# Optimization experiments

Hardware: AMD Instinct MI355X
Metric: run time of the kernel (lower is better)

Reference implementation:

```python
import jax, jax.numpy as jnp
import numpy as np

B, L, D = 4, 4096, 768

def setup_inputs() -> dict:
    key = jax.random.key(0)
    ks = jax.random.split(key, 4)
    s = 1.0 / np.sqrt(D)
    return {
        "hidden_states": jax.random.normal(ks[0], (B, L, D), dtype=jnp.float32),
        "Wq": jax.random.normal(ks[1], (D, D), dtype=jnp.float32) * s,
        "bq": jnp.zeros((D,), dtype=jnp.float32),
        "Wk": jax.random.normal(ks[2], (D, D), dtype=jnp.float32) * s,
        "bk": jnp.zeros((D,), dtype=jnp.float32),
        "Wv": jax.random.normal(ks[3], (D, D), dtype=jnp.float32) * s,
        "bv": jnp.zeros((D,), dtype=jnp.float32),
    }

def reference(hidden_states, Wq, bq, Wk, bk, Wv, bv):
    # Linear projections (torch Linear: x @ W^T + b; here W stored as [in, out]-equivalent via transpose-free einsum)
    q = jnp.einsum('bld,de->ble', hidden_states, Wq) + bq
    k = jnp.einsum('bld,de->ble', hidden_states, Wk) + bk
    v = jnp.einsum('bld,de->ble', hidden_states, Wv) + bv
    # Single-head attention, NO 1/sqrt(d) scaling (faithful to source)
    weight = jnp.einsum('bqd,bkd->bqk', q, k)          # [B, L, L]
    weight = jax.nn.softmax(weight, axis=-1)
    score = jnp.einsum('bqk,bkd->bqd', weight, v)      # [B, L, D]
    return score
```

## Files before the change

### kernel.cpp

```cpp
#include <hip/hip_runtime.h>


typedef _Float16 f16;
typedef _Float16 f16x8 __attribute__((ext_vector_type(8)));
typedef _Float16 f16x4 __attribute__((ext_vector_type(4)));
typedef float f32x4 __attribute__((ext_vector_type(4)));

#define NB 4
#define NL 4096
#define ND 768
#define NM (NB * NL)

__device__ __forceinline__ void split_f16(float v, f16& h, f16& l) {
    h = (f16)v;
    l = (f16)(v - (float)h);
}

__global__ __launch_bounds__(256) void k_convert_x(
    const float* __restrict__ x, f16* __restrict__ xh, f16* __restrict__ xl) {
    int i = blockIdx.x * 256 + threadIdx.x;
    float4 v = ((const float4*)x)[i];
    float vv[4] = {v.x, v.y, v.z, v.w};
    f16x4 hv, lv;
    for (int j = 0; j < 4; ++j) {
        f16 h, l; split_f16(vv[j], h, l);
        hv[j] = h; lv[j] = l;
    }
    ((f16x4*)xh)[i] = hv;
    ((f16x4*)xl)[i] = lv;
}

__global__ __launch_bounds__(256) void k_convert_w(
    const float* __restrict__ Wq, const float* __restrict__ Wk,
    const float* __restrict__ Wv, f16* __restrict__ wth, f16* __restrict__ wtl) {
    __shared__ float tile[32][33];
    const float* W = blockIdx.z == 0 ? Wq : (blockIdx.z == 1 ? Wk : Wv);
    f16* th = wth + blockIdx.z * ND * ND;
    f16* tl = wtl + blockIdx.z * ND * ND;
    const int k0 = blockIdx.x * 32, n0 = blockIdx.y * 32;
    const int tx = threadIdx.x & 31, ty = threadIdx.x >> 5;
    for (int r = 0; r < 4; ++r)
        tile[r * 8 + ty][tx] = W[(k0 + r * 8 + ty) * ND + n0 + tx];
    __syncthreads();
    for (int r = 0; r < 4; ++r) {
        float v = tile[tx][r * 8 + ty];
        int n = n0 + r * 8 + ty, k = k0 + tx;
        f16 h, l; split_f16(v, h, l);
        th[n * ND + k] = h;
        tl[n * ND + k] = l;
    }
}

__global__ __launch_bounds__(256, 2) void k_proj(
    const f16* __restrict__ xh, const f16* __restrict__ xl,
    const f16* __restrict__ wth, const f16* __restrict__ wtl,
    const float* __restrict__ bq, const float* __restrict__ bk,
    const float* __restrict__ bv,
    f16* __restrict__ qh, f16* __restrict__ kh, f16* __restrict__ vt) {
    const int z = blockIdx.z;
    const f16* wh = wth + z * ND * ND;
    const f16* wl = wtl + z * ND * ND;
    const float* bias = z == 0 ? bq : (z == 1 ? bk : bv);
    const int m0 = blockIdx.x * 128, n0 = blockIdx.y * 128;

    __shared__ f16 Ah[128 * 40], Al[128 * 40], Bh[128 * 40], Bl[128 * 40];

    const int t = threadIdx.x;
    const int lane = t & 63, quad = lane >> 4, l16 = lane & 15;
    const int wave = t >> 6, wm = wave >> 1, wn = wave & 1;

    f32x4 acc[4][4] = {};

    for (int kt = 0; kt < 24; ++kt) {
        const int k0 = kt * 32;
        __syncthreads();
        for (int i = 0; i < 2; ++i) {
            int c = i * 256 + t;
            int row = c >> 2, kc = (c & 3) * 8;
            *(uint4*)&Ah[row * 40 + kc] = *(const uint4*)&xh[(m0 + row) * ND + k0 + kc];
            *(uint4*)&Al[row * 40 + kc] = *(const uint4*)&xl[(m0 + row) * ND + k0 + kc];
            *(uint4*)&Bh[row * 40 + kc] = *(const uint4*)&wh[(n0 + row) * ND + k0 + kc];
            *(uint4*)&Bl[row * 40 + kc] = *(const uint4*)&wl[(n0 + row) * ND + k0 + kc];
        }
        __syncthreads();
        f16x8 ah[4], al[4], bh[4], bl[4];
#pragma unroll
        for (int f = 0; f < 4; ++f) {
            int m = wm * 64 + f * 16 + l16;
            ah[f] = *(const f16x8*)&Ah[m * 40 + quad * 8];
            al[f] = *(const f16x8*)&Al[m * 40 + quad * 8];
            int n = wn * 64 + f * 16 + l16;
            bh[f] = *(const f16x8*)&Bh[n * 40 + quad * 8];
            bl[f] = *(const f16x8*)&Bl[n * 40 + quad * 8];
        }
#pragma unroll
        for (int fm = 0; fm < 4; ++fm)
#pragma unroll
            for (int fn = 0; fn < 4; ++fn) {
                f32x4 c = acc[fm][fn];
                c = __builtin_amdgcn_mfma_f32_16x16x32_f16(al[fm], bh[fn], c, 0, 0, 0);
                c = __builtin_amdgcn_mfma_f32_16x16x32_f16(ah[fm], bl[fn], c, 0, 0, 0);
                c = __builtin_amdgcn_mfma_f32_16x16x32_f16(ah[fm], bh[fn], c, 0, 0, 0);
                acc[fm][fn] = c;
            }
    }
#pragma unroll
    for (int fm = 0; fm < 4; ++fm)
#pragma unroll
        for (int fn = 0; fn < 4; ++fn) {
            int col = n0 + wn * 64 + fn * 16 + l16;
            float bv_ = bias[col];
#pragma unroll
            for (int r = 0; r < 4; ++r) {
                int row = m0 + wm * 64 + fm * 16 + quad * 4 + r;
                float v = acc[fm][fn][r] + bv_;
                f16 h = (f16)v;
                if (z == 0) { qh[row * ND + col] = h; }
                else if (z == 1) { kh[row * ND + col] = h; }
                else {
                    int b = row >> 12, pos = row & 4095;
                    vt[(b * ND + col) * NL + pos] = h;
                }
            }
        }
}

__global__ __launch_bounds__(512) void k_attn(
    const f16* __restrict__ qh, const f16* __restrict__ kh,
    const f16* __restrict__ vt, float* __restrict__ out) {
    const int qt = blockIdx.x, b = blockIdx.y;
    const int q0 = qt * 64;
    const int t = threadIdx.x, w = t >> 6, lane = t & 63;
    const int quad = lane >> 4, l16 = lane & 15;
    const int dw = w * 96;
    const int kvw = w * 32;

    __shared__ f16 Qbuf[64 * 776];
    __shared__ f16 Pbuf[64 * 264];
    __shared__ float mwT[64][12];
    __shared__ float psT[64][12];

    const f16* kbase = &kh[((size_t)b * NL + kvw + l16) * ND];
    const f16* kbase2 = &kh[((size_t)b * NL + kvw + 16 + l16) * ND];

    for (int c = t; c < 6144; c += 512) {
        int row = c / 96, col8 = (c % 96) * 8;
        *(uint4*)&Qbuf[row * 776 + col8] =
            *(const uint4*)&qh[(b * NL + q0 + row) * ND + col8];
    }
    float mreg[4][4], lreg[4][4];
#pragma unroll
    for (int fm = 0; fm < 4; ++fm)
#pragma unroll
        for (int r = 0; r < 4; ++r) { mreg[fm][r] = -1e30f; lreg[fm][r] = 0.f; }
    f32x4 oacc[4][6] = {};
    __syncthreads();

    for (int kt = 0; kt < 16; ++kt) {
        const int p0 = kt * 256;
        const f16* kb1 = kbase + (size_t)p0 * ND;
        const f16* kb2 = kbase2 + (size_t)p0 * ND;

        f16x8 vb[2][6];
#pragma unroll
        for (int fn = 0; fn < 6; ++fn)
            vb[0][fn] = *(const f16x8*)&vt[(b * ND + dw + fn * 16 + l16) * NL +
                                           p0 + quad * 8];

        f32x4 sacc[4][2] = {};
#pragma unroll
        for (int ks = 0; ks < 24; ++ks) {
            const int d = ks * 32 + quad * 8;
            const f16x8 b0 = *(const f16x8*)&kb1[d];
            const f16x8 b1 = *(const f16x8*)&kb2[d];
#pragma unroll
            for (int fm = 0; fm < 4; ++fm) {
                f16x8 aH = *(const f16x8*)&Qbuf[(fm * 16 + l16) * 776 + d];
                sacc[fm][0] = __builtin_amdgcn_mfma_f32_16x16x32_f16(aH, b0, sacc[fm][0], 0, 0, 0);
                sacc[fm][1] = __builtin_amdgcn_mfma_f32_16x16x32_f16(aH, b1, sacc[fm][1], 0, 0, 0);
            }
        }

#pragma unroll
        for (int fm = 0; fm < 4; ++fm)
#pragma unroll
            for (int r = 0; r < 4; ++r) {
                float v = fmaxf(sacc[fm][0][r], sacc[fm][1][r]);
#pragma unroll
                for (int off = 1; off < 16; off <<= 1) v = fmaxf(v, __shfl_xor(v, off, 64));
                if (l16 == 0) mwT[fm * 16 + quad * 4 + r][w] = v;
            }
        __syncthreads();

        float alpha[4][4];
#pragma unroll
        for (int fm = 0; fm < 4; ++fm)
#pragma unroll
            for (int r = 0; r < 4; ++r) {
                const int row = fm * 16 + quad * 4 + r;
                f32x4 a4 = *(const f32x4*)&mwT[row][0];
                f32x4 b4 = *(const f32x4*)&mwT[row][4];
                float tmax = fmaxf(fmaxf(fmaxf(a4[0], a4[1]), fmaxf(a4[2], a4[3])),
                                   fmaxf(fmaxf(b4[0], b4[1]), fmaxf(b4[2], b4[3])));
                float m_new = fmaxf(mreg[fm][r], tmax);
                alpha[fm][r] = __expf(mreg[fm][r] - m_new);
                mreg[fm][r] = m_new;
                float p0v = __expf(sacc[fm][0][r] - m_new);
                float p1v = __expf(sacc[fm][1][r] - m_new);
                Pbuf[row * 264 + kvw + l16] = (f16)p0v;
                Pbuf[row * 264 + kvw + 16 + l16] = (f16)p1v;
                float ps = p0v + p1v;
#pragma unroll
                for (int off = 1; off < 16; off <<= 1) ps += __shfl_xor(ps, off, 64);
                if (l16 == 0) psT[row][w] = ps;
            }
        __syncthreads();

#pragma unroll
        for (int fm = 0; fm < 4; ++fm)
#pragma unroll
            for (int r = 0; r < 4; ++r) {
                const int row = fm * 16 + quad * 4 + r;
                f32x4 a4 = *(const f32x4*)&psT[row][0];
                f32x4 b4 = *(const f32x4*)&psT[row][4];
                lreg[fm][r] = alpha[fm][r] * lreg[fm][r] +
                              ((a4[0] + a4[1]) + (a4[2] + a4[3])) +
                              ((b4[0] + b4[1]) + (b4[2] + b4[3]));
#pragma unroll
                for (int fn = 0; fn < 6; ++fn) oacc[fm][fn][r] *= alpha[fm][r];
            }

#pragma unroll
        for (int ks = 0; ks < 8; ++ks) {
            if (ks < 7) {
#pragma unroll
                for (int fn = 0; fn < 6; ++fn)
                    vb[(ks + 1) & 1][fn] =
                        *(const f16x8*)&vt[(b * ND + dw + fn * 16 + l16) * NL +
                                           p0 + (ks + 1) * 32 + quad * 8];
            }
            f16x8 pa[4];
#pragma unroll
            for (int fm = 0; fm < 4; ++fm)
                pa[fm] = *(const f16x8*)&Pbuf[(fm * 16 + l16) * 264 + ks * 32 + quad * 8];
#pragma unroll
            for (int fn = 0; fn < 6; ++fn)
#pragma unroll
                for (int fm = 0; fm < 4; ++fm)
                    oacc[fm][fn] = __builtin_amdgcn_mfma_f32_16x16x32_f16(
                        pa[fm], vb[ks & 1][fn], oacc[fm][fn], 0, 0, 0);
        }
    }

#pragma unroll
    for (int fm = 0; fm < 4; ++fm)
#pragma unroll
        for (int fn = 0; fn < 6; ++fn) {
            int col = dw + fn * 16 + l16;
#pragma unroll
            for (int r = 0; r < 4; ++r) {
                int row = b * NL + q0 + fm * 16 + quad * 4 + r;
                out[row * ND + col] = oacc[fm][fn][r] / lreg[fm][r];
            }
        }
}

extern "C" void kernel_launch(void* const* d_in, const int* in_sizes, int n_in,
                              void* d_out, int out_size, void* d_ws, size_t ws_size,
                              hipStream_t stream) {
    const float* hs = (const float*)d_in[0];
    const float* Wq = (const float*)d_in[1];
    const float* bq = (const float*)d_in[2];
    const float* Wk = (const float*)d_in[3];
    const float* bk = (const float*)d_in[4];
    const float* Wv = (const float*)d_in[5];
    const float* bv = (const float*)d_in[6];
    float* out = (float*)d_out;

    char* ws = (char*)d_ws;
    size_t off = 0;
    auto alloc = [&](size_t bytes) {
        void* p = ws + off;
        off += (bytes + 255) & ~(size_t)255;
        return p;
    };
    const size_t MD = (size_t)NM * ND;
    f16* Xh = (f16*)alloc(MD * 2);
    f16* Xl = (f16*)alloc(MD * 2);
    f16* Wth = (f16*)alloc((size_t)3 * ND * ND * 2);
    f16* Wtl = (f16*)alloc((size_t)3 * ND * ND * 2);
    f16* Qh = (f16*)alloc(MD * 2);
    f16* Kh = (f16*)alloc(MD * 2);
    f16* Vt = (f16*)alloc(MD * 2);
    (void)ws_size; (void)in_sizes; (void)n_in; (void)out_size;

    k_convert_x<<<dim3(MD / 1024), 256, 0, stream>>>(hs, Xh, Xl);
    k_convert_w<<<dim3(24, 24, 3), 256, 0, stream>>>(Wq, Wk, Wv, Wth, Wtl);
    k_proj<<<dim3(NM / 128, ND / 128, 3), 256, 0, stream>>>(
        Xh, Xl, Wth, Wtl, bq, bk, bv, Qh, Kh, Vt);
    k_attn<<<dim3(NL / 64, NB), 512, 0, stream>>>(Qh, Kh, Vt, out);
}
```

Before: 842.1 us.

## Move softmax running max/sum to shared memory and batch K loads

Moves the per-row running max and sum out of per-thread registers into double-buffered shared arrays, updated by a single wave, to cut register pressure in the attention kernel. The QK^T loop is restructured to load four K fragments at once before issuing the MFMAs, so more global loads are in flight. This adds shared-memory reads per tile and a final barrier, and raises live registers for the batched K fragments. The double-buffered state relies on the existing barriers for ordering.

```diff
diff --git a/kernel.cpp b/kernel.cpp
--- a/kernel.cpp
+++ b/kernel.cpp
@@ -139,6 +139,8 @@
     __shared__ f16 Pbuf[64 * 264];
     __shared__ float mwT[64][12];
     __shared__ float psT[64][12];
+    __shared__ float mstate[2][64];
+    __shared__ float lstate[2][64];
 
     const f16* kbase = &kh[((size_t)b * NL + kvw + l16) * ND];
     const f16* kbase2 = &kh[((size_t)b * NL + kvw + 16 + l16) * ND];
@@ -148,16 +150,13 @@
         *(uint4*)&Qbuf[row * 776 + col8] =
             *(const uint4*)&qh[(b * NL + q0 + row) * ND + col8];
     }
-    float mreg[4][4], lreg[4][4];
-#pragma unroll
-    for (int fm = 0; fm < 4; ++fm)
-#pragma unroll
-        for (int r = 0; r < 4; ++r) { mreg[fm][r] = -1e30f; lreg[fm][r] = 0.f; }
+    if (t < 64) { mstate[0][t] = -1e30f; lstate[0][t] = 0.f; }
     f32x4 oacc[4][6] = {};
     __syncthreads();
 
     for (int kt = 0; kt < 16; ++kt) {
         const int p0 = kt * 256;
+        const int cb = kt & 1;
         const f16* kb1 = kbase + (size_t)p0 * ND;
         const f16* kb2 = kbase2 + (size_t)p0 * ND;
 
@@ -169,15 +168,23 @@
 
         f32x4 sacc[4][2] = {};
 #pragma unroll
-        for (int ks = 0; ks < 24; ++ks) {
-            const int d = ks * 32 + quad * 8;
-            const f16x8 b0 = *(const f16x8*)&kb1[d];
-            const f16x8 b1 = *(const f16x8*)&kb2[d];
-#pragma unroll
-            for (int fm = 0; fm < 4; ++fm) {
-                f16x8 aH = *(const f16x8*)&Qbuf[(fm * 16 + l16) * 776 + d];
-                sacc[fm][0] = __builtin_amdgcn_mfma_f32_16x16x32_f16(aH, b0, sacc[fm][0], 0, 0, 0);
-                sacc[fm][1] = __builtin_amdgcn_mfma_f32_16x16x32_f16(aH, b1, sacc[fm][1], 0, 0, 0);
+        for (int g = 0; g < 6; ++g) {
+            f16x8 kA[4], kB[4];
+#pragma unroll
+            for (int i = 0; i < 4; ++i) {
+                const int d = (g * 4 + i) * 32 + quad * 8;
+                kA[i] = *(const f16x8*)&kb1[d];
+                kB[i] = *(const f16x8*)&kb2[d];
+            }
+#pragma unroll
+            for (int i = 0; i < 4; ++i) {
+                const int d = (g * 4 + i) * 32 + quad * 8;
+#pragma unroll
+                for (int fm = 0; fm < 4; ++fm) {
+                    f16x8 aH = *(const f16x8*)&Qbuf[(fm * 16 + l16) * 776 + d];
+                    sacc[fm][0] = __builtin_amdgcn_mfma_f32_16x16x32_f16(aH, kA[i], sacc[fm][0], 0, 0, 0);
+                    sacc[fm][1] = __builtin_amdgcn_mfma_f32_16x16x32_f16(aH, kB[i], sacc[fm][1], 0, 0, 0);
+                }
             }
         }
 
@@ -202,9 +209,10 @@
                 f32x4 b4 = *(const f32x4*)&mwT[row][4];
                 float tmax = fmaxf(fmaxf(fmaxf(a4[0], a4[1]), fmaxf(a4[2], a4[3])),
                                    fmaxf(fmaxf(b4[0], b4[1]), fmaxf(b4[2], b4[3])));
-                float m_new = fmaxf(mreg[fm][r], tmax);
-                alpha[fm][r] = __expf(mreg[fm][r] - m_new);
-                mreg[fm][r] = m_new;
+                float m_old = mstate[cb][row];
+                float m_new = fmaxf(m_old, tmax);
+                alpha[fm][r] = __expf(m_old - m_new);
+                if (w == 0 && l16 == 0) mstate[cb ^ 1][row] = m_new;
                 float p0v = __expf(sacc[fm][0][r] - m_new);
                 float p1v = __expf(sacc[fm][1][r] - m_new);
                 Pbuf[row * 264 + kvw + l16] = (f16)p0v;
@@ -221,11 +229,13 @@
 #pragma unroll
             for (int r = 0; r < 4; ++r) {
                 const int row = fm * 16 + quad * 4 + r;
-                f32x4 a4 = *(const f32x4*)&psT[row][0];
-                f32x4 b4 = *(const f32x4*)&psT[row][4];
-                lreg[fm][r] = alpha[fm][r] * lreg[fm][r] +
-                              ((a4[0] + a4[1]) + (a4[2] + a4[3])) +
-                              ((b4[0] + b4[1]) + (b4[2] + b4[3]));
+                if (w == 0 && l16 == 0) {
+                    f32x4 a4 = *(const f32x4*)&psT[row][0];
+                    f32x4 b4 = *(const f32x4*)&psT[row][4];
+                    lstate[cb ^ 1][row] = alpha[fm][r] * lstate[cb][row] +
+                                          ((a4[0] + a4[1]) + (a4[2] + a4[3])) +
+                                          ((b4[0] + b4[1]) + (b4[2] + b4[3]));
+                }
 #pragma unroll
                 for (int fn = 0; fn < 6; ++fn) oacc[fm][fn][r] *= alpha[fm][r];
             }
@@ -252,6 +262,7 @@
         }
     }
 
+    __syncthreads();
 #pragma unroll
     for (int fm = 0; fm < 4; ++fm)
 #pragma unroll
@@ -260,7 +271,8 @@
 #pragma unroll
             for (int r = 0; r < 4; ++r) {
                 int row = b * NL + q0 + fm * 16 + quad * 4 + r;
-                out[row * ND + col] = oacc[fm][fn][r] / lreg[fm][r];
+                out[row * ND + col] =
+                    oacc[fm][fn][r] / lstate[0][fm * 16 + quad * 4 + r];
             }
         }
 }
```

Result: faster. 763.4 us (-9.3%).
